# Kernel tuning notes

Hardware: AMD Instinct MI355X
Metric: run time of the kernel (lower is better)

## Reference

```python
import jax, jax.numpy as jnp
import numpy as np


def setup_inputs() -> dict:
    key = jax.random.key(0)
    k1, k2 = jax.random.split(key)
    N, M, Q, D = 4096, 128, 64, 128
    a_embeddings = jax.random.normal(k1, (N, D), dtype=jnp.float32)
    b_embedding_sets = jax.random.normal(k2, (M, Q, D), dtype=jnp.float32)
    gaussian_variance = jnp.full((1,), 0.5, dtype=jnp.float32)  # nn.Parameter default
    return {
        "a_embeddings": a_embeddings,
        "b_embedding_sets": b_embedding_sets,
        "gaussian_variance": gaussian_variance,
    }


def reference(a_embeddings, b_embedding_sets, gaussian_variance):
    # Covariance = var * I, so inv(cov) = I / var and the Mahalanobis term is
    # ||a - mu||^2 / var. Expand the squared distance to avoid the NxMxQxD
    # broadcast intermediate the torch code materializes (same math).
    inv_var = 1.0 / gaussian_variance[0]
    a2 = jnp.sum(a_embeddings * a_embeddings, axis=-1)          # [N]
    b2 = jnp.sum(b_embedding_sets * b_embedding_sets, axis=-1)  # [M, Q]
    ab = jnp.einsum("nd,mqd->nmq", a_embeddings, b_embedding_sets)  # [N, M, Q]
    x2 = (a2[:, None, None] - 2.0 * ab + b2[None, :, :]) * inv_var  # [N, M, Q]
    densities = jnp.exp(-0.5 * x2)                  # [N, M, Q]
    dens_per_cluster = densities.sum(axis=2)        # [N, M]
    prob = dens_per_cluster / (dens_per_cluster.sum(axis=1, keepdims=True) + 1e-10)
    return prob
```

## Files before the change

### kernel.cpp

```cpp
#include <hip/hip_runtime.h>
#include <math.h>

#define NN 4096
#define MM 128
#define QQ 64
#define DD 128
#define CC (MM * QQ)

typedef float f32x4 __attribute__((ext_vector_type(4)));
typedef int   i32x4 __attribute__((ext_vector_type(4)));
typedef int   i32x8 __attribute__((ext_vector_type(8)));

#define AS1 __attribute__((address_space(1)))
#define AS3 __attribute__((address_space(3)))

__global__ __launch_bounds__(256)
void prep_kernel(const float* __restrict__ A, const float* __restrict__ B,
                 unsigned char* __restrict__ A8, unsigned char* __restrict__ B8,
                 float* __restrict__ a2, float* __restrict__ b2)
{
    const int row = blockIdx.x * 8 + (threadIdx.x >> 5);
    const int l32 = threadIdx.x & 31;
    const float* src;
    unsigned char* dst;
    float* nrm;
    if (row < NN) { src = A + (size_t)row * DD; dst = A8 + (size_t)row * DD; nrm = a2 + row; }
    else {
        int r = row - NN;
        src = B + (size_t)r * DD; dst = B8 + (size_t)r * DD; nrm = b2 + r;
    }
    float4 v = ((const float4*)src)[l32];
    int pk = __builtin_amdgcn_cvt_pk_fp8_f32(v.x, v.y, 0, false);
    pk     = __builtin_amdgcn_cvt_pk_fp8_f32(v.z, v.w, pk, true);
    ((int*)dst)[l32] = pk;
    float s = v.x * v.x + v.y * v.y + v.z * v.z + v.w * v.w;
    #pragma unroll
    for (int m = 16; m > 0; m >>= 1) s += __shfl_xor(s, m, 64);
    if (l32 == 0) *nrm = s;
}

__global__ __launch_bounds__(256, 3)
void kde_dens_kernel(const unsigned char* __restrict__ A8,
                     const unsigned char* __restrict__ B8,
                     const float* __restrict__ var,
                     const float* __restrict__ a2w,
                     const float* __restrict__ b2w,
                     float* __restrict__ dpc)
{
    __shared__ unsigned char As[128 * DD];
    __shared__ unsigned char Bs[128 * DD];
    __shared__ float a2s[128];
    __shared__ float b2s[128];

    const int lin = blockIdx.x;
    const int xcd = lin & 7;
    const int loc = lin >> 3;
    const int cb  = (xcd << 3) | (loc & 7);
    const int nb  = loc >> 3;
    const int n0  = nb * 128;
    const int c0  = cb * 128;

    const int t = threadIdx.x, w = t >> 6, lane = t & 63;

    {
        const unsigned char* Ab = A8 + (size_t)n0 * DD;
        const unsigned char* Bb = B8 + (size_t)c0 * DD;
        #pragma unroll
        for (int i = 0; i < 4; ++i) {
            const int slot = w * 256 + i * 64 + lane;
            const int r = slot >> 3, c16 = slot & 7, scb = c16 ^ (r & 7);
            __builtin_amdgcn_global_load_lds(
                (const AS1 unsigned int*)(Ab + r * DD + scb * 16),
                (AS3 unsigned int*)&As[slot * 16], 16, 0, 0);
            __builtin_amdgcn_global_load_lds(
                (const AS1 unsigned int*)(Bb + r * DD + scb * 16),
                (AS3 unsigned int*)&Bs[slot * 16], 16, 0, 0);
        }
        if (t < 128)        a2s[t]       = a2w[n0 + t];
        else                b2s[t - 128] = b2w[c0 + (t - 128)];
    }
    __syncthreads();

    const int l15 = lane & 15, q = lane >> 4, xr = l15 & 7;
    const int wy = w >> 1, wx = w & 1;
    const int rbase = wy * 64, cbase = wx * 64;
    const int m = (cb << 1) + wx;
    const float hinvL = (0.5f / var[0]) * 1.44269504088896f;
    const float h2L   = hinvL + hinvL;

    f32x4 nbh[4];
    i32x8 b8v[4];
    #pragma unroll
    for (int jc = 0; jc < 4; ++jc) {
        const f32x4 bv = *(const f32x4*)&b2s[cbase + jc * 16 + q * 4];
        nbh[jc] = -bv * hinvL;
        const int ro = (cbase + jc * 16 + l15) * DD;
        const i32x4 lo = *(const i32x4*)&Bs[ro + (((q << 1) | 0) ^ xr) * 16];
        const i32x4 hi = *(const i32x4*)&Bs[ro + (((q << 1) | 1) ^ xr) * 16];
        #pragma unroll
        for (int e = 0; e < 4; ++e) { b8v[jc][e] = lo[e]; b8v[jc][4 + e] = hi[e]; }
    }

    i32x8 a8[4];
    #pragma unroll
    for (int i = 0; i < 4; ++i) {
        const int ro = (rbase + i * 16 + l15) * DD;
        const i32x4 lo = *(const i32x4*)&As[ro + (((q << 1) | 0) ^ xr) * 16];
        const i32x4 hi = *(const i32x4*)&As[ro + (((q << 1) | 1) ^ xr) * 16];
        #pragma unroll
        for (int e = 0; e < 4; ++e) { a8[i][e] = lo[e]; a8[i][4 + e] = hi[e]; }
    }

    f32x4 acc[4][4] = {};
    __builtin_amdgcn_s_setprio(1);
    #pragma unroll
    for (int jc = 0; jc < 4; ++jc)
        #pragma unroll
        for (int i = 0; i < 4; ++i)
            acc[jc][i] = __builtin_amdgcn_mfma_scale_f32_16x16x128_f8f6f4(
                            b8v[jc], a8[i], acc[jc][i],
                            0, 0,
                            0, 127,
                            0, 127);
    __builtin_amdgcn_s_setprio(0);

    float sums[4];
    #pragma unroll
    for (int i = 0; i < 4; ++i) {
        const float aih = a2s[rbase + i * 16 + l15] * hinvL;
        float s0 = 0.f, s1 = 0.f;
        #pragma unroll
        for (int jc = 0; jc < 4; jc += 2) {
            #pragma unroll
            for (int r = 0; r < 4; ++r) {
                s0 += __builtin_amdgcn_exp2f(fmaf(h2L, acc[jc][i][r],     nbh[jc][r]     - aih));
                s1 += __builtin_amdgcn_exp2f(fmaf(h2L, acc[jc + 1][i][r], nbh[jc + 1][r] - aih));
            }
        }
        float s = s0 + s1;
        s += __shfl_xor(s, 16, 64);
        s += __shfl_xor(s, 32, 64);
        sums[i] = s;
    }
    const float v01 = (q & 1) ? sums[1] : sums[0];
    const float v23 = (q & 1) ? sums[3] : sums[2];
    const float myv = (q & 2) ? v23 : v01;
    dpc[(size_t)m * NN + n0 + rbase + lane] = myv;
}

__global__ __launch_bounds__(256)
void kde_norm_kernel(const float* __restrict__ dpc, float* __restrict__ out)
{
    __shared__ float tile[128][17];
    __shared__ float rden[16];
    const int n0 = blockIdx.x * 16;
    const int t  = threadIdx.x;

    const int mr = t >> 1, half = t & 1;
    {
        const float4 va = *(const float4*)&dpc[(size_t)mr * NN + n0 + half * 8];
        const float4 vb = *(const float4*)&dpc[(size_t)mr * NN + n0 + half * 8 + 4];
        float* tr = &tile[mr][half * 8];
        tr[0] = va.x; tr[1] = va.y; tr[2] = va.z; tr[3] = va.w;
        tr[4] = vb.x; tr[5] = vb.y; tr[6] = vb.z; tr[7] = vb.w;
    }
    __syncthreads();

    if (t < 16) {
        float s = 0.f;
        #pragma unroll 8
        for (int mm = 0; mm < MM; ++mm) s += tile[mm][t];
        rden[t] = 1.f / (s + 1e-10f);
    }
    __syncthreads();

    const int j = t >> 4, m0 = (t & 15) * 8;
    const float r = rden[j];
    float4 o0, o1;
    o0.x = tile[m0][j] * r;     o0.y = tile[m0 + 1][j] * r;
    o0.z = tile[m0 + 2][j] * r; o0.w = tile[m0 + 3][j] * r;
    o1.x = tile[m0 + 4][j] * r; o1.y = tile[m0 + 5][j] * r;
    o1.z = tile[m0 + 6][j] * r; o1.w = tile[m0 + 7][j] * r;
    float* obase = &out[(size_t)(n0 + j) * MM + m0];
    *(float4*)obase       = o0;
    *(float4*)(obase + 4) = o1;
}

extern "C" void kernel_launch(void* const* d_in, const int* in_sizes, int n_in,
                              void* d_out, int out_size, void* d_ws, size_t ws_size,
                              hipStream_t stream) {
    const float* A   = (const float*)d_in[0];
    const float* B   = (const float*)d_in[1];
    const float* var = (const float*)d_in[2];
    float* out = (float*)d_out;

    unsigned char* A8 = (unsigned char*)d_ws;
    unsigned char* B8 = A8 + (size_t)NN * DD;
    float* a2  = (float*)(B8 + (size_t)CC * DD);
    float* b2  = a2 + NN;
    float* dpc = b2 + CC;

    prep_kernel<<<(NN + CC) / 8, 256, 0, stream>>>(A, B, A8, B8, a2, b2);
    kde_dens_kernel<<<2048, 256, 0, stream>>>(A8, B8, var, a2, b2, dpc);
    kde_norm_kernel<<<NN / 16, 256, 0, stream>>>(dpc, out);
}
```

Baseline: 76.80 us.

## Process two A row tiles per block to reuse loaded B fragments

Each density block now covers 256 A rows instead of 128. It loads both A tiles into LDS and loops twice over the MFMA and exp stages while keeping the B fragments in registers. This halves the grid and halves the B tile reloads from global memory. The cost is more LDS per block and the removal of the occupancy hint and the setprio calls, which may lower occupancy and the overlap between waves.

```diff
diff --git a/kernel.cpp b/kernel.cpp
--- a/kernel.cpp
+++ b/kernel.cpp
@@ -39,7 +39,7 @@
     if (l32 == 0) *nrm = s;
 }
 
-__global__ __launch_bounds__(256, 3)
+__global__ __launch_bounds__(256)
 void kde_dens_kernel(const unsigned char* __restrict__ A8,
                      const unsigned char* __restrict__ B8,
                      const float* __restrict__ var,
@@ -47,17 +47,17 @@
                      const float* __restrict__ b2w,
                      float* __restrict__ dpc)
 {
-    __shared__ unsigned char As[128 * DD];
+    __shared__ unsigned char As[2 * 128 * DD];
     __shared__ unsigned char Bs[128 * DD];
-    __shared__ float a2s[128];
+    __shared__ float a2s[256];
     __shared__ float b2s[128];
 
     const int lin = blockIdx.x;
     const int xcd = lin & 7;
     const int loc = lin >> 3;
     const int cb  = (xcd << 3) | (loc & 7);
-    const int nb  = loc >> 3;
-    const int n0  = nb * 128;
+    const int nb2 = loc >> 3;
+    const int n0  = nb2 * 256;
     const int c0  = cb * 128;
 
     const int t = threadIdx.x, w = t >> 6, lane = t & 63;
@@ -65,19 +65,25 @@
     {
         const unsigned char* Ab = A8 + (size_t)n0 * DD;
         const unsigned char* Bb = B8 + (size_t)c0 * DD;
+        #pragma unroll
+        for (int i = 0; i < 8; ++i) {
+            const int slot = w * 512 + i * 64 + lane;
+            const int r = slot >> 3;
+            const int c16 = slot & 7, scb = c16 ^ (r & 7);
+            __builtin_amdgcn_global_load_lds(
+                (const AS1 unsigned int*)(Ab + (size_t)r * DD + scb * 16),
+                (AS3 unsigned int*)&As[slot * 16], 16, 0, 0);
+        }
         #pragma unroll
         for (int i = 0; i < 4; ++i) {
             const int slot = w * 256 + i * 64 + lane;
             const int r = slot >> 3, c16 = slot & 7, scb = c16 ^ (r & 7);
             __builtin_amdgcn_global_load_lds(
-                (const AS1 unsigned int*)(Ab + r * DD + scb * 16),
-                (AS3 unsigned int*)&As[slot * 16], 16, 0, 0);
-            __builtin_amdgcn_global_load_lds(
-                (const AS1 unsigned int*)(Bb + r * DD + scb * 16),
+                (const AS1 unsigned int*)(Bb + (size_t)r * DD + scb * 16),
                 (AS3 unsigned int*)&Bs[slot * 16], 16, 0, 0);
         }
-        if (t < 128)        a2s[t]       = a2w[n0 + t];
-        else                b2s[t - 128] = b2w[c0 + (t - 128)];
+        a2s[t] = a2w[n0 + t];
+        if (t < 128) b2s[t] = b2w[c0 + t];
     }
     __syncthreads();
 
@@ -101,51 +107,52 @@
         for (int e = 0; e < 4; ++e) { b8v[jc][e] = lo[e]; b8v[jc][4 + e] = hi[e]; }
     }
 
-    i32x8 a8[4];
     #pragma unroll
-    for (int i = 0; i < 4; ++i) {
-        const int ro = (rbase + i * 16 + l15) * DD;
-        const i32x4 lo = *(const i32x4*)&As[ro + (((q << 1) | 0) ^ xr) * 16];
-        const i32x4 hi = *(const i32x4*)&As[ro + (((q << 1) | 1) ^ xr) * 16];
-        #pragma unroll
-        for (int e = 0; e < 4; ++e) { a8[i][e] = lo[e]; a8[i][4 + e] = hi[e]; }
-    }
-
-    f32x4 acc[4][4] = {};
-    __builtin_amdgcn_s_setprio(1);
-    #pragma unroll
-    for (int jc = 0; jc < 4; ++jc)
-        #pragma unroll
-        for (int i = 0; i < 4; ++i)
-            acc[jc][i] = __builtin_amdgcn_mfma_scale_f32_16x16x128_f8f6f4(
-                            b8v[jc], a8[i], acc[jc][i],
-                            0, 0,
-                            0, 127,
-                            0, 127);
-    __builtin_amdgcn_s_setprio(0);
-
-    float sums[4];
-    #pragma unroll
-    for (int i = 0; i < 4; ++i) {
-        const float aih = a2s[rbase + i * 16 + l15] * hinvL;
-        float s0 = 0.f, s1 = 0.f;
-        #pragma unroll
-        for (int jc = 0; jc < 4; jc += 2) {
+    for (int t4 = 0; t4 < 2; ++t4) {
+        i32x8 a8[4];
+        #pragma unroll
+        for (int i = 0; i < 4; ++i) {
+            const int ro = ((t4 << 7) + rbase + i * 16 + l15) * DD;
+            const i32x4 lo = *(const i32x4*)&As[ro + (((q << 1) | 0) ^ xr) * 16];
+            const i32x4 hi = *(const i32x4*)&As[ro + (((q << 1) | 1) ^ xr) * 16];
             #pragma unroll
-            for (int r = 0; r < 4; ++r) {
-                s0 += __builtin_amdgcn_exp2f(fmaf(h2L, acc[jc][i][r],     nbh[jc][r]     - aih));
-                s1 += __builtin_amdgcn_exp2f(fmaf(h2L, acc[jc + 1][i][r], nbh[jc + 1][r] - aih));
+            for (int e = 0; e < 4; ++e) { a8[i][e] = lo[e]; a8[i][4 + e] = hi[e]; }
+        }
+
+        f32x4 acc[4][4] = {};
+        #pragma unroll
+        for (int jc = 0; jc < 4; ++jc)
+            #pragma unroll
+            for (int i = 0; i < 4; ++i)
+                acc[jc][i] = __builtin_amdgcn_mfma_scale_f32_16x16x128_f8f6f4(
+                                b8v[jc], a8[i], acc[jc][i],
+                                0, 0,
+                                0, 127,
+                                0, 127);
+
+        float sums[4];
+        #pragma unroll
+        for (int i = 0; i < 4; ++i) {
+            const float aih = a2s[(t4 << 7) + rbase + i * 16 + l15] * hinvL;
+            float s0 = 0.f, s1 = 0.f;
+            #pragma unroll
+            for (int jc = 0; jc < 4; jc += 2) {
+                #pragma unroll
+                for (int r = 0; r < 4; ++r) {
+                    s0 += __builtin_amdgcn_exp2f(fmaf(h2L, acc[jc][i][r],     nbh[jc][r]     - aih));
+                    s1 += __builtin_amdgcn_exp2f(fmaf(h2L, acc[jc + 1][i][r], nbh[jc + 1][r] - aih));
+                }
             }
-        }
-        float s = s0 + s1;
-        s += __shfl_xor(s, 16, 64);
-        s += __shfl_xor(s, 32, 64);
-        sums[i] = s;
-    }
-    const float v01 = (q & 1) ? sums[1] : sums[0];
-    const float v23 = (q & 1) ? sums[3] : sums[2];
-    const float myv = (q & 2) ? v23 : v01;
-    dpc[(size_t)m * NN + n0 + rbase + lane] = myv;
+            float s = s0 + s1;
+            s += __shfl_xor(s, 16, 64);
+            s += __shfl_xor(s, 32, 64);
+            sums[i] = s;
+        }
+        const float v01 = (q & 1) ? sums[1] : sums[0];
+        const float v23 = (q & 1) ? sums[3] : sums[2];
+        const float myv = (q & 2) ? v23 : v01;
+        dpc[(size_t)m * NN + n0 + (t4 << 7) + rbase + lane] = myv;
+    }
 }
 
 __global__ __launch_bounds__(256)
@@ -201,6 +208,6 @@
     float* dpc = b2 + CC;
 
     prep_kernel<<<(NN + CC) / 8, 256, 0, stream>>>(A, B, A8, B8, a2, b2);
-    kde_dens_kernel<<<2048, 256, 0, stream>>>(A8, B8, var, a2, b2, dpc);
+    kde_dens_kernel<<<1024, 256, 0, stream>>>(A8, B8, var, a2, b2, dpc);
     kde_norm_kernel<<<NN / 16, 256, 0, stream>>>(dpc, out);
 }
```

Result: no change. 77.15 us (+0.5%).

## Accumulate row denominators via atomics and load norms directly into registers

Applied to the files above, without the earlier changes.

The density kernel now atomically adds each per-cluster sum into a per-row denominator buffer, which the prep kernel zeroes. This removes the serial 128-element column reduction and one barrier from the normalize kernel. The a2/b2 norm values are also read straight from global memory into registers before the LDS loads, instead of being staged through shared memory. In exchange, the density kernel issues 4096x128 float atomics to 4096 addresses, which adds contention and makes the summation order nondeterministic.

```diff
diff --git a/kernel.cpp b/kernel.cpp
--- a/kernel.cpp
+++ b/kernel.cpp
@@ -17,8 +17,11 @@
 __global__ __launch_bounds__(256)
 void prep_kernel(const float* __restrict__ A, const float* __restrict__ B,
                  unsigned char* __restrict__ A8, unsigned char* __restrict__ B8,
-                 float* __restrict__ a2, float* __restrict__ b2)
+                 float* __restrict__ a2, float* __restrict__ b2,
+                 float* __restrict__ den)
 {
+    if (blockIdx.x < 16) den[blockIdx.x * 256 + threadIdx.x] = 0.f;
+
     const int row = blockIdx.x * 8 + (threadIdx.x >> 5);
     const int l32 = threadIdx.x & 31;
     const float* src;
@@ -45,12 +48,11 @@
                      const float* __restrict__ var,
                      const float* __restrict__ a2w,
                      const float* __restrict__ b2w,
-                     float* __restrict__ dpc)
+                     float* __restrict__ dpc,
+                     float* __restrict__ den)
 {
     __shared__ unsigned char As[128 * DD];
     __shared__ unsigned char Bs[128 * DD];
-    __shared__ float a2s[128];
-    __shared__ float b2s[128];
 
     const int lin = blockIdx.x;
     const int xcd = lin & 7;
@@ -61,6 +63,22 @@
     const int c0  = cb * 128;
 
     const int t = threadIdx.x, w = t >> 6, lane = t & 63;
+    const int l15 = lane & 15, q = lane >> 4, xr = l15 & 7;
+    const int wy = w >> 1, wx = w & 1;
+    const int rbase = wy * 64, cbase = wx * 64;
+    const int m = (cb << 1) + wx;
+
+    const float hinvL = (0.5f / var[0]) * 1.44269504088896f;
+    const float h2L   = hinvL + hinvL;
+    float a2r[4];
+    #pragma unroll
+    for (int i = 0; i < 4; ++i) a2r[i] = a2w[n0 + rbase + i * 16 + l15];
+    f32x4 nbh[4];
+    #pragma unroll
+    for (int jc = 0; jc < 4; ++jc) {
+        const f32x4 bv = *(const f32x4*)&b2w[c0 + cbase + jc * 16 + q * 4];
+        nbh[jc] = -bv * hinvL;
+    }
 
     {
         const unsigned char* Ab = A8 + (size_t)n0 * DD;
@@ -76,24 +94,12 @@
                 (const AS1 unsigned int*)(Bb + r * DD + scb * 16),
                 (AS3 unsigned int*)&Bs[slot * 16], 16, 0, 0);
         }
-        if (t < 128)        a2s[t]       = a2w[n0 + t];
-        else                b2s[t - 128] = b2w[c0 + (t - 128)];
     }
     __syncthreads();
 
-    const int l15 = lane & 15, q = lane >> 4, xr = l15 & 7;
-    const int wy = w >> 1, wx = w & 1;
-    const int rbase = wy * 64, cbase = wx * 64;
-    const int m = (cb << 1) + wx;
-    const float hinvL = (0.5f / var[0]) * 1.44269504088896f;
-    const float h2L   = hinvL + hinvL;
-
-    f32x4 nbh[4];
     i32x8 b8v[4];
     #pragma unroll
     for (int jc = 0; jc < 4; ++jc) {
-        const f32x4 bv = *(const f32x4*)&b2s[cbase + jc * 16 + q * 4];
-        nbh[jc] = -bv * hinvL;
         const int ro = (cbase + jc * 16 + l15) * DD;
         const i32x4 lo = *(const i32x4*)&Bs[ro + (((q << 1) | 0) ^ xr) * 16];
         const i32x4 hi = *(const i32x4*)&Bs[ro + (((q << 1) | 1) ^ xr) * 16];
@@ -127,7 +133,7 @@
     float sums[4];
     #pragma unroll
     for (int i = 0; i < 4; ++i) {
-        const float aih = a2s[rbase + i * 16 + l15] * hinvL;
+        const float aih = a2r[i] * hinvL;
         float s0 = 0.f, s1 = 0.f;
         #pragma unroll
         for (int jc = 0; jc < 4; jc += 2) {
@@ -146,15 +152,19 @@
     const float v23 = (q & 1) ? sums[3] : sums[2];
     const float myv = (q & 2) ? v23 : v01;
     dpc[(size_t)m * NN + n0 + rbase + lane] = myv;
+    atomicAdd(&den[n0 + rbase + lane], myv);
 }
 
 __global__ __launch_bounds__(256)
-void kde_norm_kernel(const float* __restrict__ dpc, float* __restrict__ out)
+void kde_norm_kernel(const float* __restrict__ dpc, const float* __restrict__ den,
+                     float* __restrict__ out)
 {
     __shared__ float tile[128][17];
     __shared__ float rden[16];
     const int n0 = blockIdx.x * 16;
     const int t  = threadIdx.x;
+
+    if (t < 16) rden[t] = 1.f / (den[n0 + t] + 1e-10f);
 
     const int mr = t >> 1, half = t & 1;
     {
@@ -163,14 +173,6 @@
         float* tr = &tile[mr][half * 8];
         tr[0] = va.x; tr[1] = va.y; tr[2] = va.z; tr[3] = va.w;
         tr[4] = vb.x; tr[5] = vb.y; tr[6] = vb.z; tr[7] = vb.w;
-    }
-    __syncthreads();
-
-    if (t < 16) {
-        float s = 0.f;
-        #pragma unroll 8
-        for (int mm = 0; mm < MM; ++mm) s += tile[mm][t];
-        rden[t] = 1.f / (s + 1e-10f);
     }
     __syncthreads();
 
@@ -198,9 +200,10 @@
     unsigned char* B8 = A8 + (size_t)NN * DD;
     float* a2  = (float*)(B8 + (size_t)CC * DD);
     float* b2  = a2 + NN;
-    float* dpc = b2 + CC;
-
-    prep_kernel<<<(NN + CC) / 8, 256, 0, stream>>>(A, B, A8, B8, a2, b2);
-    kde_dens_kernel<<<2048, 256, 0, stream>>>(A8, B8, var, a2, b2, dpc);
-    kde_norm_kernel<<<NN / 16, 256, 0, stream>>>(dpc, out);
-}
+    float* den = b2 + CC;
+    float* dpc = den + NN;
+
+    prep_kernel<<<(NN + CC) / 8, 256, 0, stream>>>(A, B, A8, B8, a2, b2, den);
+    kde_dens_kernel<<<2048, 256, 0, stream>>>(A8, B8, var, a2, b2, dpc, den);
+    kde_norm_kernel<<<NN / 16, 256, 0, stream>>>(dpc, den, out);
+}
```

Measured after the change: 82.00 us. 6.8% more time.
